# Optimization experiments

Hardware: AMD Instinct MI355X
Metric: run time of the kernel (lower is better)

The kernel has to match this reference:

```python
import jax, jax.numpy as jnp
import numpy as np

N = 50000      # nodes
E = 800000     # edges per relation
R = 4          # relations
F = 256        # feature_size
H = 128        # hid_dim
O = 32         # out_dim
B = 10000      # batch_nodes
EPS = 1e-5


def setup_inputs() -> dict:
    key = jax.random.key(0)
    ks = jax.random.split(key, 12)
    features = jax.random.normal(ks[0], (N, F), dtype=jnp.float32)
    multi_r_edge_index = jax.random.randint(ks[1], (R, 2, E), 0, N, dtype=jnp.int64)
    batch_nodes = jax.random.randint(ks[2], (B,), 0, N, dtype=jnp.int64)
    # per-relation params, stacked on leading R axis
    W1 = jax.random.normal(ks[3], (R, F, H), dtype=jnp.float32) / np.sqrt(F)
    b1 = jnp.zeros((R, H), dtype=jnp.float32)
    g1 = jnp.ones((R, H), dtype=jnp.float32)
    be1 = jnp.zeros((R, H), dtype=jnp.float32)
    W2 = jax.random.normal(ks[4], (R, H, O), dtype=jnp.float32) / np.sqrt(H)
    b2 = jnp.zeros((R, O), dtype=jnp.float32)
    g2 = jnp.ones((R, O), dtype=jnp.float32)
    be2 = jnp.zeros((R, O), dtype=jnp.float32)
    return {"features": features, "multi_r_edge_index": multi_r_edge_index,
            "batch_nodes": batch_nodes, "W1": W1, "b1": b1, "g1": g1, "be1": be1,
            "W2": W2, "b2": b2, "g2": g2, "be2": be2}


def gcn_conv(x, src, dst, W, b):
    # PyG GCNConv: h = x W; add self-loops; sym-norm aggregate; + bias
    h = x @ W                                   # [N, D]
    loops = jnp.arange(N, dtype=src.dtype)
    s = jnp.concatenate([src, loops])
    d = jnp.concatenate([dst, loops])
    deg = jax.ops.segment_sum(jnp.ones_like(d, dtype=h.dtype), d, num_segments=N)
    dinv = jnp.where(deg > 0, jax.lax.rsqrt(deg), 0.0)
    norm = dinv[s] * dinv[d]                    # [E+N]
    msgs = norm[:, None] * h[s]                 # gather [E+N, D]
    out = jax.ops.segment_sum(msgs, d, num_segments=N)  # scatter
    return out + b


def batchnorm(x, gamma, beta):
    # training-mode batch stats over node dim (biased variance)
    mean = jnp.mean(x, axis=0)
    var = jnp.mean(jnp.square(x - mean), axis=0)
    return gamma * (x - mean) * jax.lax.rsqrt(var + EPS) + beta


def reference(features, multi_r_edge_index, batch_nodes, W1, b1, g1, be1, W2, b2, g2, be2):
    embeds = []
    for i in range(R):  # small fixed loop over relations
        src = multi_r_edge_index[i, 0]
        dst = multi_r_edge_index[i, 1]
        x = gcn_conv(features, src, dst, W1[i], b1[i])
        x = jax.nn.relu(batchnorm(x, g1[i], be1[i]))
        # dropout: eval mode (identity)
        x = gcn_conv(x, src, dst, W2[i], b2[i])
        x = jax.nn.relu(batchnorm(x, g2[i], be2[i]))
        embeds.append(jax.nn.log_softmax(x[batch_nodes], axis=1))  # [B, O]
    multi = jnp.stack(embeds, axis=1)            # [B, R, O]
    return multi.reshape(B, R * O)
```

## Files before the change

kernel.cpp:

```cpp
#include <hip/hip_runtime.h>
#include <math.h>

#define NN 50000
#define EE 800000
#define RR 4
#define FF 256
#define HH 128
#define OO 32
#define BB 10000
#define EPSV 1e-5f
#define PAIR 2

#define NSEG 256
#define CH   (EE / NSEG)
#define NBK  256
#define BNODE 196
#define SCAP 36

typedef __bf16 bf16_t;
typedef __attribute__((ext_vector_type(8))) bf16_t bf16x8;
typedef __attribute__((ext_vector_type(4))) float f32x4;

__device__ __forceinline__ unsigned short f2bf(float f) {
    unsigned int u = __float_as_uint(f);
    u += 0x7fff + ((u >> 16) & 1);
    return (unsigned short)(u >> 16);
}
__device__ __forceinline__ float bf2f(unsigned short s) {
    return __uint_as_float(((unsigned int)s) << 16);
}
__device__ __forceinline__ void load_lds16(const void* g, void* l) {
    __builtin_amdgcn_global_load_lds(
        (const __attribute__((address_space(1))) unsigned int*)g,
        (__attribute__((address_space(3))) unsigned int*)l, 16, 0, 0);
}


__global__ void k_cvt_feat(const float* __restrict__ in, ushort* __restrict__ out) {
    int idx = blockIdx.x * 256 + threadIdx.x;
    const float4* p = (const float4*)in + (size_t)idx * 2;
    float4 a = p[0], b = p[1];
    uint4 o;
    o.x = (unsigned)f2bf(a.x) | ((unsigned)f2bf(a.y) << 16);
    o.y = (unsigned)f2bf(a.z) | ((unsigned)f2bf(a.w) << 16);
    o.z = (unsigned)f2bf(b.x) | ((unsigned)f2bf(b.y) << 16);
    o.w = (unsigned)f2bf(b.z) | ((unsigned)f2bf(b.w) << 16);
    ((uint4*)out)[idx] = o;
}

__global__ void k_cvt_w(const float* __restrict__ W1, const float* __restrict__ W2,
                        ushort* __restrict__ W1t, ushort* __restrict__ W2t) {
    int idx = blockIdx.x * 256 + threadIdx.x;
    if (idx < RR * FF * HH) {
        int r = idx >> 15, k = (idx >> 7) & 255, n = idx & 127;
        W1t[r * (HH * FF) + n * FF + k] = f2bf(W1[idx]);
    }
    if (idx < RR * HH * OO) {
        int r = idx >> 12, k = (idx >> 5) & 127, n = idx & 31;
        W2t[r * (OO * HH) + n * HH + k] = f2bf(W2[idx]);
    }
}


__global__ __launch_bounds__(256) void k_passA(const int* __restrict__ edges,
                                               uint* __restrict__ seg,
                                               int* __restrict__ cnt) {
    int r = blockIdx.y, blk = blockIdx.x, t = threadIdx.x;
    __shared__ int lcur[NBK];
    lcur[t] = 0;
    __syncthreads();
    const int* srcp = edges + (size_t)r * 2 * EE + blk * CH;
    const int* dstp = srcp + EE;
    uint* segbase = seg + (size_t)(r * NSEG + blk) * NBK * SCAP;
    for (int i = t; i < CH; i += 256) {
        int s = srcp[i], d = dstp[i];
        int b = d / BNODE;
        int dloc = d - b * BNODE;
        int pos = atomicAdd(&lcur[b], 1);
        if (pos < SCAP) segbase[b * SCAP + pos] = (uint)s | ((uint)dloc << 16);
    }
    __syncthreads();
    cnt[(r * NSEG + blk) * NBK + t] = min(lcur[t], SCAP);
}

__global__ void k_bbase(const int* __restrict__ cnt, int* __restrict__ bbase,
                        int* __restrict__ offs) {
    int r = blockIdx.x, t = threadIdx.x;
    int sum = 0;
    for (int s = 0; s < NSEG; ++s) sum += cnt[(r * NSEG + s) * NBK + t];
    __shared__ int sh[256];
    sh[t] = sum;
    __syncthreads();
    for (int off = 1; off < 256; off <<= 1) {
        int u = (t >= off) ? sh[t - off] : 0;
        __syncthreads();
        sh[t] += u;
        __syncthreads();
    }
    bbase[r * (NBK + 1) + t] = sh[t] - sum;
    if (t == 255) {
        bbase[r * (NBK + 1) + NBK] = sh[t];
        offs[r * (NN + 1) + NN] = sh[t];
    }
}

__global__ __launch_bounds__(256) void k_passB(const uint* __restrict__ seg,
                                               const int* __restrict__ cnt,
                                               const int* __restrict__ bbase,
                                               ushort* __restrict__ csr,
                                               int* __restrict__ offs,
                                               float* __restrict__ dinv) {
    int b = blockIdx.x, r = blockIdx.y, t = threadIdx.x;
    __shared__ int ldeg[256];
    __shared__ int lcur[256];
    __shared__ int sh[256];
    __shared__ int scnt[NSEG];
    ldeg[t] = 0;
    scnt[t] = cnt[(r * NSEG + t) * NBK + b];
    __syncthreads();
    const uint* segb = seg + (size_t)(r * NSEG) * NBK * SCAP + (size_t)b * SCAP;
    for (int idx = t; idx < NSEG * SCAP; idx += 256) {
        int s = idx / SCAP, i = idx - s * SCAP;
        if (i < scnt[s])
            atomicAdd(&ldeg[segb[(size_t)s * NBK * SCAP + i] >> 16], 1);
    }
    __syncthreads();
    int v = ldeg[t];
    sh[t] = v;
    __syncthreads();
    for (int off = 1; off < 256; off <<= 1) {
        int u = (t >= off) ? sh[t - off] : 0;
        __syncthreads();
        sh[t] += u;
        __syncthreads();
    }
    int ex = sh[t] - v;
    lcur[t] = ex;
    int gbase = bbase[r * (NBK + 1) + b];
    int n0 = b * BNODE;
    int n = n0 + t;
    if (t < BNODE && n < NN) {
        offs[r * (NN + 1) + n] = gbase + ex;
        dinv[r * NN + n] = rsqrtf((float)(v + 1));
    }
    __syncthreads();
    ushort* csrb = csr + (size_t)r * EE + gbase;
    for (int idx = t; idx < NSEG * SCAP; idx += 256) {
        int s = idx / SCAP, i = idx - s * SCAP;
        if (i < scnt[s]) {
            uint e = segb[(size_t)s * NBK * SCAP + i];
            int p = atomicAdd(&lcur[e >> 16], 1);
            csrb[p] = (ushort)(e & 0xffffu);
        }
    }
}


__global__ __launch_bounds__(256) void k_mm1(const ushort* __restrict__ A,
                                             const ushort* __restrict__ W1t_all,
                                             ushort* __restrict__ C_all, int rbase) {
    int pr = blockIdx.y, r = rbase + pr;
    const ushort* Wt = W1t_all + (size_t)r * FF * HH;
    ushort* C = C_all + (size_t)pr * NN * HH;
    __shared__ __align__(16) ushort As[128 * 32];
    __shared__ __align__(16) ushort Bs[128 * 32];
    int tid = threadIdx.x;
    int lane = tid & 63, w = tid >> 6;
    int wm = w >> 1, wn = w & 1;
    int row0 = blockIdx.x * 128;
    int l15 = lane & 15, l4 = lane >> 4;

    f32x4 acc[4][4];
#pragma unroll
    for (int mf = 0; mf < 4; ++mf)
#pragma unroll
        for (int nf = 0; nf < 4; ++nf) acc[mf][nf] = (f32x4)0.f;

    for (int k0 = 0; k0 < FF; k0 += 32) {
#pragma unroll
        for (int i = 0; i < 2; ++i) {
            int chunk = i * 256 + tid;
            int ar = chunk >> 2, as_ = chunk & 3;
            int grow = row0 + ar; if (grow > NN - 1) grow = NN - 1;
            load_lds16(A + (size_t)grow * FF + k0 + as_ * 8,
                       As + (size_t)(i * 256 + w * 64) * 8);
        }
#pragma unroll
        for (int i = 0; i < 2; ++i) {
            int chunk = i * 256 + tid;
            int bn = chunk >> 2, slot = chunk & 3;
            uint4 v = *(const uint4*)(Wt + bn * FF + k0 + slot * 8);
            int sw = slot ^ ((bn >> 1) & 3);
            *(uint4*)(Bs + bn * 32 + sw * 8) = v;
        }
        __syncthreads();
        bf16x8 af[4], bfr[4];
#pragma unroll
        for (int mf = 0; mf < 4; ++mf) {
            int row = wm * 64 + mf * 16 + l15;
            af[mf] = *(const bf16x8*)(As + row * 32 + l4 * 8);
        }
#pragma unroll
        for (int nf = 0; nf < 4; ++nf) {
            int n = wn * 64 + nf * 16 + l15;
            int sw = l4 ^ ((n >> 1) & 3);
            bfr[nf] = *(const bf16x8*)(Bs + n * 32 + sw * 8);
        }
#pragma unroll
        for (int mf = 0; mf < 4; ++mf)
#pragma unroll
            for (int nf = 0; nf < 4; ++nf)
                acc[mf][nf] = __builtin_amdgcn_mfma_f32_16x16x32_bf16(af[mf], bfr[nf], acc[mf][nf], 0, 0, 0);
        __syncthreads();
    }
#pragma unroll
    for (int mf = 0; mf < 4; ++mf) {
#pragma unroll
        for (int nf = 0; nf < 4; ++nf) {
#pragma unroll
            for (int j = 0; j < 4; ++j) {
                int row = row0 + wm * 64 + mf * 16 + l4 * 4 + j;
                if (row < NN)
                    C[(size_t)row * HH + wn * 64 + nf * 16 + l15] = f2bf(acc[mf][nf][j]);
            }
        }
    }
}


__global__ __launch_bounds__(256) void k_mm2(const ushort* __restrict__ A_all,
                                             const float* __restrict__ ab_all,
                                             const ushort* __restrict__ W2t_all,
                                             ushort* __restrict__ C_all, int rbase) {
    int pr = blockIdx.y, r = rbase + pr;
    const ushort* A = A_all + (size_t)pr * NN * HH;
    const float* ab = ab_all + pr * 2 * HH;
    const ushort* Wt = W2t_all + (size_t)r * OO * HH;
    ushort* C = C_all + (size_t)pr * NN * OO;
    __shared__ __align__(16) ushort As[256 * 32];
    __shared__ __align__(16) ushort Ws2[32 * 128];
    int tid = threadIdx.x;
    int lane = tid & 63, w = tid >> 6;
    int l15 = lane & 15, l4 = lane >> 4;
    int row0 = blockIdx.x * 256;

#pragma unroll
    for (int i = 0; i < 2; ++i) {
        int chunk = i * 256 + tid;
        int n = chunk >> 4, slot = chunk & 15;
        uint4 v = *(const uint4*)(Wt + n * HH + slot * 8);
        int sw = slot ^ (n & 7);
        *(uint4*)(Ws2 + n * HH + sw * 8) = v;
    }

    f32x4 acc[4][2];
#pragma unroll
    for (int mf = 0; mf < 4; ++mf)
#pragma unroll
        for (int nf = 0; nf < 2; ++nf) acc[mf][nf] = (f32x4)0.f;

    for (int k0 = 0; k0 < HH; k0 += 32) {
#pragma unroll
        for (int i = 0; i < 4; ++i) {
            int chunk = i * 256 + tid;
            int ar = chunk >> 2, cg = chunk & 3;
            int grow = row0 + ar; if (grow > NN - 1) grow = NN - 1;
            uint4 xv = *(const uint4*)(A + (size_t)grow * HH + k0 + cg * 8);
            const float* aa = ab + k0 + cg * 8;
            float4 a0 = *(const float4*)aa;
            float4 a1 = *(const float4*)(aa + 4);
            const float* bp = ab + HH + k0 + cg * 8;
            float4 b0 = *(const float4*)bp;
            float4 b1 = *(const float4*)(bp + 4);
            float y0 = fmaxf(a0.x * bf2f((ushort)(xv.x & 0xffff)) + b0.x, 0.f);
            float y1 = fmaxf(a0.y * bf2f((ushort)(xv.x >> 16)) + b0.y, 0.f);
            float y2 = fmaxf(a0.z * bf2f((ushort)(xv.y & 0xffff)) + b0.z, 0.f);
            float y3 = fmaxf(a0.w * bf2f((ushort)(xv.y >> 16)) + b0.w, 0.f);
            float y4 = fmaxf(a1.x * bf2f((ushort)(xv.z & 0xffff)) + b1.x, 0.f);
            float y5 = fmaxf(a1.y * bf2f((ushort)(xv.z >> 16)) + b1.y, 0.f);
            float y6 = fmaxf(a1.z * bf2f((ushort)(xv.w & 0xffff)) + b1.z, 0.f);
            float y7 = fmaxf(a1.w * bf2f((ushort)(xv.w >> 16)) + b1.w, 0.f);
            uint4 o;
            o.x = (unsigned)f2bf(y0) | ((unsigned)f2bf(y1) << 16);
            o.y = (unsigned)f2bf(y2) | ((unsigned)f2bf(y3) << 16);
            o.z = (unsigned)f2bf(y4) | ((unsigned)f2bf(y5) << 16);
            o.w = (unsigned)f2bf(y6) | ((unsigned)f2bf(y7) << 16);
            *(uint4*)(As + chunk * 8) = o;
        }
        __syncthreads();
        bf16x8 af[4], bfr[2];
#pragma unroll
        for (int mf = 0; mf < 4; ++mf)
            af[mf] = *(const bf16x8*)(As + (w * 64 + mf * 16 + l15) * 32 + l4 * 8);
#pragma unroll
        for (int nf = 0; nf < 2; ++nf) {
            int n = nf * 16 + l15;
            int slot = (k0 >> 3) + l4;
            int sw = slot ^ (n & 7);
            bfr[nf] = *(const bf16x8*)(Ws2 + n * HH + sw * 8);
        }
#pragma unroll
        for (int mf = 0; mf < 4; ++mf)
#pragma unroll
            for (int nf = 0; nf < 2; ++nf)
                acc[mf][nf] = __builtin_amdgcn_mfma_f32_16x16x32_bf16(af[mf], bfr[nf], acc[mf][nf], 0, 0, 0);
        __syncthreads();
    }
#pragma unroll
    for (int mf = 0; mf < 4; ++mf) {
#pragma unroll
        for (int nf = 0; nf < 2; ++nf) {
#pragma unroll
            for (int j = 0; j < 4; ++j) {
                int row = row0 + w * 64 + mf * 16 + l4 * 4 + j;
                if (row < NN)
                    C[(size_t)row * OO + nf * 16 + l15] = f2bf(acc[mf][nf][j]);
            }
        }
    }
}


__global__ void k_agg1(const ushort* __restrict__ X_all, ushort* __restrict__ Y_all,
                       const int* __restrict__ offs_all, const ushort* __restrict__ csr_all,
                       const float* __restrict__ dinv_all, int rbase) {
    int pr = blockIdx.y, r = rbase + pr;
    const uint* Xu = (const uint*)(X_all + (size_t)pr * NN * HH);
    uint* Yu = (uint*)(Y_all + (size_t)pr * NN * HH);
    const int* offs = offs_all + r * (NN + 1);
    const ushort* csr = csr_all + (size_t)r * EE;
    const float* dinv = dinv_all + (size_t)r * NN;
    int tid = threadIdx.x;
    int wid = tid >> 6, lane = tid & 63;
    int n = blockIdx.x * 4 + wid;
    if (n >= NN) return;
    float ax = 0.f, ay = 0.f;
    int e = offs[n], s1 = offs[n + 1];
    for (; e + 4 <= s1; e += 4) {
        int sa = csr[e], sb = csr[e + 1], sc = csr[e + 2], sd = csr[e + 3];
        uint va = Xu[sa * 64 + lane];
        uint vb = Xu[sb * 64 + lane];
        uint vc = Xu[sc * 64 + lane];
        uint vd = Xu[sd * 64 + lane];
        float wa = dinv[sa], wb = dinv[sb], wc = dinv[sc], wd = dinv[sd];
        ax += wa * bf2f((ushort)(va & 0xffff)); ay += wa * bf2f((ushort)(va >> 16));
        ax += wb * bf2f((ushort)(vb & 0xffff)); ay += wb * bf2f((ushort)(vb >> 16));
        ax += wc * bf2f((ushort)(vc & 0xffff)); ay += wc * bf2f((ushort)(vc >> 16));
        ax += wd * bf2f((ushort)(vd & 0xffff)); ay += wd * bf2f((ushort)(vd >> 16));
    }
    for (; e < s1; ++e) {
        int s = csr[e];
        float w = dinv[s];
        uint v = Xu[s * 64 + lane];
        ax += w * bf2f((ushort)(v & 0xffff)); ay += w * bf2f((ushort)(v >> 16));
    }
    float dn = dinv[n];
    uint v = Xu[n * 64 + lane];
    ax += dn * bf2f((ushort)(v & 0xffff));
    ay += dn * bf2f((ushort)(v >> 16));
    Yu[n * 64 + lane] = (uint)f2bf(ax * dn) | ((uint)f2bf(ay * dn) << 16);
}

__global__ void k_agg2(const ushort* __restrict__ X_all, ushort* __restrict__ Y_all,
                       const int* __restrict__ offs_all, const ushort* __restrict__ csr_all,
                       const float* __restrict__ dinv_all, int rbase) {
    int pr = blockIdx.y, r = rbase + pr;
    const ushort* X = X_all + (size_t)pr * NN * OO;
    ushort* Y = Y_all + (size_t)pr * NN * OO;
    const int* offs = offs_all + r * (NN + 1);
    const ushort* csr = csr_all + (size_t)r * EE;
    const float* dinv = dinv_all + (size_t)r * NN;
    int tid = threadIdx.x;
    int wid = tid >> 6, lane = tid & 63;
    int sub = lane >> 5, col = lane & 31;
    int n = blockIdx.x * 8 + wid * 2 + sub;
    if (n >= NN) return;
    float acc = 0.f;
    int e = offs[n], s1 = offs[n + 1];
    for (; e + 4 <= s1; e += 4) {
        int sa = csr[e], sb = csr[e + 1], sc = csr[e + 2], sd = csr[e + 3];
        float xa = bf2f(X[sa * OO + col]);
        float xb = bf2f(X[sb * OO + col]);
        float xc = bf2f(X[sc * OO + col]);
        float xd = bf2f(X[sd * OO + col]);
        acc += dinv[sa] * xa + dinv[sb] * xb + dinv[sc] * xc + dinv[sd] * xd;
    }
    for (; e < s1; ++e) {
        int s = csr[e];
        acc += dinv[s] * bf2f(X[s * OO + col]);
    }
    float dn = dinv[n];
    acc += dn * bf2f(X[n * OO + col]);
    Y[(size_t)n * OO + col] = f2bf(acc * dn);
}


template <int D>
__global__ void k_stats(const ushort* __restrict__ X_all, float* __restrict__ partial_all) {
    constexpr int BY = 256 / D;
    int pr = blockIdx.y;
    const ushort* X = X_all + (size_t)pr * NN * D;
    float* partial = partial_all + (size_t)pr * 256 * 2 * D;
    int c = threadIdx.x;
    int ty = threadIdx.y;
    float s = 0.f, ss = 0.f;
    for (int row = blockIdx.x * BY + ty; row < NN; row += 256 * BY) {
        float v = bf2f(X[(size_t)row * D + c]);
        s += v; ss += v * v;
    }
    __shared__ float ls[BY][D];
    __shared__ float lss[BY][D];
    ls[ty][c] = s; lss[ty][c] = ss;
    __syncthreads();
    if (ty == 0) {
#pragma unroll
        for (int y = 1; y < BY; ++y) { s += ls[y][c]; ss += lss[y][c]; }
        partial[blockIdx.x * 2 * D + c] = s;
        partial[blockIdx.x * 2 * D + D + c] = ss;
    }
}

template <int D>
__global__ void k_finalize(const float* __restrict__ partial_all, const float* __restrict__ g_all,
                           const float* __restrict__ be_all, float* __restrict__ ab_all, int rbase) {
    int pr = blockIdx.x, r = rbase + pr;
    const float* partial = partial_all + (size_t)pr * 256 * 2 * D;
    int c = threadIdx.x;
    float s = 0.f, ss = 0.f;
    for (int i = 0; i < 256; ++i) {
        s += partial[i * 2 * D + c];
        ss += partial[i * 2 * D + D + c];
    }
    float mean = s / (float)NN;
    float var = ss / (float)NN - mean * mean;
    float rstd = rsqrtf(var + EPSV);
    float a = g_all[r * D + c] * rstd;
    ab_all[pr * 2 * D + c] = a;
    ab_all[pr * 2 * D + D + c] = be_all[r * D + c] - mean * a;
}


__global__ void k_lsm(const ushort* __restrict__ X_all, const float* __restrict__ ab_all,
                      const int* __restrict__ batch, float* __restrict__ out, int rbase) {
    int pr = blockIdx.y, r = rbase + pr;
    const ushort* X = X_all + (size_t)pr * NN * OO;
    const float* ab = ab_all + pr * 2 * OO;
    int tx = threadIdx.x;
    int b = blockIdx.x * blockDim.y + threadIdx.y;
    if (b >= BB) return;
    int node = batch[b];
    float x = bf2f(X[(size_t)node * OO + tx]);
    float v = fmaxf(ab[tx] * x + ab[OO + tx], 0.f);
    float m = v;
#pragma unroll
    for (int off = 16; off; off >>= 1) m = fmaxf(m, __shfl_xor(m, off, 32));
    float e = expf(v - m);
    float sum = e;
#pragma unroll
    for (int off = 16; off; off >>= 1) sum += __shfl_xor(sum, off, 32);
    out[(size_t)b * (RR * OO) + r * OO + tx] = v - m - logf(sum);
}


extern "C" void kernel_launch(void* const* d_in, const int* in_sizes, int n_in,
                              void* d_out, int out_size, void* d_ws, size_t ws_size,
                              hipStream_t stream) {
    const float* features = (const float*)d_in[0];
    const int* edges = (const int*)d_in[1];
    const int* batch = (const int*)d_in[2];
    const float* W1 = (const float*)d_in[3];
    const float* g1 = (const float*)d_in[5];
    const float* be1 = (const float*)d_in[6];
    const float* W2 = (const float*)d_in[7];
    const float* g2 = (const float*)d_in[9];
    const float* be2 = (const float*)d_in[10];
    float* out = (float*)d_out;

    char* p = (char*)d_ws;
    auto carve = [&](size_t bytes) {
        void* q = (void*)p;
        p += (bytes + 255) & ~(size_t)255;
        return q;
    };
    ushort* Fbf = (ushort*)carve((size_t)NN * FF * 2);
    ushort* W1t = (ushort*)carve((size_t)RR * FF * HH * 2);
    ushort* W2t = (ushort*)carve((size_t)RR * HH * OO * 2);
    float* dinv = (float*)carve((size_t)RR * NN * 4);
    int* offs = (int*)carve((size_t)RR * (NN + 1) * 4);
    int* cnt = (int*)carve((size_t)RR * NSEG * NBK * 4);
    int* bbase = (int*)carve((size_t)RR * (NBK + 1) * 4);
    ushort* csr = (ushort*)carve((size_t)RR * EE * 2);
    ushort* bufAh = (ushort*)carve((size_t)PAIR * NN * HH * 2);
    ushort* bufB = (ushort*)carve((size_t)PAIR * NN * HH * 2);
    ushort* bufCh = (ushort*)carve((size_t)PAIR * NN * OO * 2);
    ushort* bufD = (ushort*)carve((size_t)PAIR * NN * OO * 2);
    float* partial = (float*)carve((size_t)PAIR * 256 * 2 * HH * 4);
    float* ab1 = (float*)carve((size_t)PAIR * 2 * HH * 4);
    float* ab2 = (float*)carve((size_t)PAIR * 2 * OO * 4);
    uint* seg = (uint*)bufAh;

    k_cvt_feat<<<NN * FF / 8 / 256, 256, 0, stream>>>(features, Fbf);
    k_cvt_w<<<(RR * FF * HH + 255) / 256, 256, 0, stream>>>(W1, W2, W1t, W2t);

    k_passA<<<dim3(NSEG, RR), 256, 0, stream>>>(edges, seg, cnt);
    k_bbase<<<RR, 256, 0, stream>>>(cnt, bbase, offs);
    k_passB<<<dim3(NBK, RR), 256, 0, stream>>>(seg, cnt, bbase, csr, offs, dinv);

    for (int rbase = 0; rbase < RR; rbase += PAIR) {
        k_mm1<<<dim3((NN + 127) / 128, PAIR), 256, 0, stream>>>(Fbf, W1t, bufAh, rbase);
        k_agg1<<<dim3((NN + 3) / 4, PAIR), 256, 0, stream>>>(bufAh, bufB, offs, csr, dinv, rbase);
        k_stats<HH><<<dim3(256, PAIR), dim3(HH, 2), 0, stream>>>(bufB, partial);
        k_finalize<HH><<<PAIR, HH, 0, stream>>>(partial, g1, be1, ab1, rbase);

        k_mm2<<<dim3((NN + 255) / 256, PAIR), 256, 0, stream>>>(bufB, ab1, W2t, bufCh, rbase);
        k_agg2<<<dim3((NN + 7) / 8, PAIR), 256, 0, stream>>>(bufCh, bufD, offs, csr, dinv, rbase);
        k_stats<OO><<<dim3(256, PAIR), dim3(OO, 8), 0, stream>>>(bufD, partial);
        k_finalize<OO><<<PAIR, OO, 0, stream>>>(partial, g2, be2, ab2, rbase);

        k_lsm<<<dim3((BB + 7) / 8, PAIR), dim3(32, 8), 0, stream>>>(bufD, ab2, batch, out, rbase);
    }
}
```

Before: 636.5 us.

## Process all relations at once when workspace allows, unroll gathers, vectorize stats

When the workspace is large enough, all four relations are processed in a single batch instead of two pairs. This halves the number of kernel launches and makes each grid larger, and the layer-2 buffers reuse the bf16 feature buffer once it is no longer needed. The aggregation kernels now gather eight neighbors per iteration to raise memory-level parallelism. The batch-norm stats kernel reads two bf16 values per 32-bit load. The larger batch needs more workspace and falls back to pairs otherwise; aliasing Fbf is only safe if k_mm1 for every relation has already run, which holds only when all four run in one batch.

```diff
diff --git a/kernel.cpp b/kernel.cpp
--- a/kernel.cpp
+++ b/kernel.cpp
@@ -9,7 +9,6 @@
 #define OO 32
 #define BB 10000
 #define EPSV 1e-5f
-#define PAIR 2
 
 #define NSEG 256
 #define CH   (EE / NSEG)
@@ -336,13 +335,29 @@
     if (n >= NN) return;
     float ax = 0.f, ay = 0.f;
     int e = offs[n], s1 = offs[n + 1];
+    for (; e + 8 <= s1; e += 8) {
+        int ia = csr[e], ib = csr[e + 1], ic = csr[e + 2], id = csr[e + 3];
+        int ie = csr[e + 4], if_ = csr[e + 5], ig = csr[e + 6], ih = csr[e + 7];
+        uint va = Xu[ia * 64 + lane], vb = Xu[ib * 64 + lane];
+        uint vc = Xu[ic * 64 + lane], vd = Xu[id * 64 + lane];
+        uint ve = Xu[ie * 64 + lane], vf = Xu[if_ * 64 + lane];
+        uint vg = Xu[ig * 64 + lane], vh = Xu[ih * 64 + lane];
+        float wa = dinv[ia], wb = dinv[ib], wc = dinv[ic], wd = dinv[id];
+        float we = dinv[ie], wf = dinv[if_], wg = dinv[ig], wh = dinv[ih];
+        ax += wa * bf2f((ushort)(va & 0xffff)); ay += wa * bf2f((ushort)(va >> 16));
+        ax += wb * bf2f((ushort)(vb & 0xffff)); ay += wb * bf2f((ushort)(vb >> 16));
+        ax += wc * bf2f((ushort)(vc & 0xffff)); ay += wc * bf2f((ushort)(vc >> 16));
+        ax += wd * bf2f((ushort)(vd & 0xffff)); ay += wd * bf2f((ushort)(vd >> 16));
+        ax += we * bf2f((ushort)(ve & 0xffff)); ay += we * bf2f((ushort)(ve >> 16));
+        ax += wf * bf2f((ushort)(vf & 0xffff)); ay += wf * bf2f((ushort)(vf >> 16));
+        ax += wg * bf2f((ushort)(vg & 0xffff)); ay += wg * bf2f((ushort)(vg >> 16));
+        ax += wh * bf2f((ushort)(vh & 0xffff)); ay += wh * bf2f((ushort)(vh >> 16));
+    }
     for (; e + 4 <= s1; e += 4) {
-        int sa = csr[e], sb = csr[e + 1], sc = csr[e + 2], sd = csr[e + 3];
-        uint va = Xu[sa * 64 + lane];
-        uint vb = Xu[sb * 64 + lane];
-        uint vc = Xu[sc * 64 + lane];
-        uint vd = Xu[sd * 64 + lane];
-        float wa = dinv[sa], wb = dinv[sb], wc = dinv[sc], wd = dinv[sd];
+        int ia = csr[e], ib = csr[e + 1], ic = csr[e + 2], id = csr[e + 3];
+        uint va = Xu[ia * 64 + lane], vb = Xu[ib * 64 + lane];
+        uint vc = Xu[ic * 64 + lane], vd = Xu[id * 64 + lane];
+        float wa = dinv[ia], wb = dinv[ib], wc = dinv[ic], wd = dinv[id];
         ax += wa * bf2f((ushort)(va & 0xffff)); ay += wa * bf2f((ushort)(va >> 16));
         ax += wb * bf2f((ushort)(vb & 0xffff)); ay += wb * bf2f((ushort)(vb >> 16));
         ax += wc * bf2f((ushort)(vc & 0xffff)); ay += wc * bf2f((ushort)(vc >> 16));
@@ -377,13 +392,21 @@
     if (n >= NN) return;
     float acc = 0.f;
     int e = offs[n], s1 = offs[n + 1];
+    for (; e + 8 <= s1; e += 8) {
+        int ia = csr[e], ib = csr[e + 1], ic = csr[e + 2], id = csr[e + 3];
+        int ie = csr[e + 4], if_ = csr[e + 5], ig = csr[e + 6], ih = csr[e + 7];
+        float xa = bf2f(X[ia * OO + col]), xb = bf2f(X[ib * OO + col]);
+        float xc = bf2f(X[ic * OO + col]), xd = bf2f(X[id * OO + col]);
+        float xe = bf2f(X[ie * OO + col]), xf = bf2f(X[if_ * OO + col]);
+        float xg = bf2f(X[ig * OO + col]), xh = bf2f(X[ih * OO + col]);
+        acc += dinv[ia] * xa + dinv[ib] * xb + dinv[ic] * xc + dinv[id] * xd;
+        acc += dinv[ie] * xe + dinv[if_] * xf + dinv[ig] * xg + dinv[ih] * xh;
+    }
     for (; e + 4 <= s1; e += 4) {
-        int sa = csr[e], sb = csr[e + 1], sc = csr[e + 2], sd = csr[e + 3];
-        float xa = bf2f(X[sa * OO + col]);
-        float xb = bf2f(X[sb * OO + col]);
-        float xc = bf2f(X[sc * OO + col]);
-        float xd = bf2f(X[sd * OO + col]);
-        acc += dinv[sa] * xa + dinv[sb] * xb + dinv[sc] * xc + dinv[sd] * xd;
+        int ia = csr[e], ib = csr[e + 1], ic = csr[e + 2], id = csr[e + 3];
+        float xa = bf2f(X[ia * OO + col]), xb = bf2f(X[ib * OO + col]);
+        float xc = bf2f(X[ic * OO + col]), xd = bf2f(X[id * OO + col]);
+        acc += dinv[ia] * xa + dinv[ib] * xb + dinv[ic] * xc + dinv[id] * xd;
     }
     for (; e < s1; ++e) {
         int s = csr[e];
@@ -397,26 +420,34 @@
 
 template <int D>
 __global__ void k_stats(const ushort* __restrict__ X_all, float* __restrict__ partial_all) {
-    constexpr int BY = 256 / D;
+    constexpr int CW = D / 2;
+    constexpr int BY = 512 / D;
     int pr = blockIdx.y;
-    const ushort* X = X_all + (size_t)pr * NN * D;
+    const uint* X = (const uint*)(X_all + (size_t)pr * NN * D);
     float* partial = partial_all + (size_t)pr * 256 * 2 * D;
     int c = threadIdx.x;
     int ty = threadIdx.y;
-    float s = 0.f, ss = 0.f;
+    float s0 = 0.f, ss0 = 0.f, s1 = 0.f, ss1 = 0.f;
     for (int row = blockIdx.x * BY + ty; row < NN; row += 256 * BY) {
-        float v = bf2f(X[(size_t)row * D + c]);
-        s += v; ss += v * v;
-    }
-    __shared__ float ls[BY][D];
-    __shared__ float lss[BY][D];
-    ls[ty][c] = s; lss[ty][c] = ss;
+        uint v = X[(size_t)row * CW + c];
+        float a = bf2f((ushort)(v & 0xffff)), b = bf2f((ushort)(v >> 16));
+        s0 += a; ss0 += a * a; s1 += b; ss1 += b * b;
+    }
+    __shared__ float ls[BY][2][CW];
+    __shared__ float lss[BY][2][CW];
+    ls[ty][0][c] = s0; ls[ty][1][c] = s1;
+    lss[ty][0][c] = ss0; lss[ty][1][c] = ss1;
     __syncthreads();
     if (ty == 0) {
 #pragma unroll
-        for (int y = 1; y < BY; ++y) { s += ls[y][c]; ss += lss[y][c]; }
-        partial[blockIdx.x * 2 * D + c] = s;
-        partial[blockIdx.x * 2 * D + D + c] = ss;
+        for (int y = 1; y < BY; ++y) {
+            s0 += ls[y][0][c]; s1 += ls[y][1][c];
+            ss0 += lss[y][0][c]; ss1 += lss[y][1][c];
+        }
+        partial[blockIdx.x * 2 * D + 2 * c] = s0;
+        partial[blockIdx.x * 2 * D + 2 * c + 1] = s1;
+        partial[blockIdx.x * 2 * D + D + 2 * c] = ss0;
+        partial[blockIdx.x * 2 * D + D + 2 * c + 1] = ss1;
     }
 }
 
@@ -490,13 +521,25 @@
     int* cnt = (int*)carve((size_t)RR * NSEG * NBK * 4);
     int* bbase = (int*)carve((size_t)RR * (NBK + 1) * 4);
     ushort* csr = (ushort*)carve((size_t)RR * EE * 2);
-    ushort* bufAh = (ushort*)carve((size_t)PAIR * NN * HH * 2);
-    ushort* bufB = (ushort*)carve((size_t)PAIR * NN * HH * 2);
-    ushort* bufCh = (ushort*)carve((size_t)PAIR * NN * OO * 2);
-    ushort* bufD = (ushort*)carve((size_t)PAIR * NN * OO * 2);
-    float* partial = (float*)carve((size_t)PAIR * 256 * 2 * HH * 4);
-    float* ab1 = (float*)carve((size_t)PAIR * 2 * HH * 4);
-    float* ab2 = (float*)carve((size_t)PAIR * 2 * OO * 4);
+
+    size_t fixed = (size_t)(p - (char*)d_ws);
+    size_t need4 = fixed + 2 * (size_t)4 * NN * HH * 2 + (size_t)4 * 256 * 2 * HH * 4 + (1 << 20);
+    int PR = (ws_size >= need4) ? 4 : 2;
+
+    ushort* bufAh = (ushort*)carve((size_t)PR * NN * HH * 2);
+    ushort* bufB = (ushort*)carve((size_t)PR * NN * HH * 2);
+    ushort* bufCh;
+    ushort* bufD;
+    if (PR == 4) {
+        bufCh = Fbf;
+        bufD = Fbf + (size_t)4 * NN * OO;
+    } else {
+        bufCh = (ushort*)carve((size_t)PR * NN * OO * 2);
+        bufD = (ushort*)carve((size_t)PR * NN * OO * 2);
+    }
+    float* partial = (float*)carve((size_t)PR * 256 * 2 * HH * 4);
+    float* ab1 = (float*)carve((size_t)PR * 2 * HH * 4);
+    float* ab2 = (float*)carve((size_t)PR * 2 * OO * 4);
     uint* seg = (uint*)bufAh;
 
     k_cvt_feat<<<NN * FF / 8 / 256, 256, 0, stream>>>(features, Fbf);
@@ -506,17 +549,17 @@
     k_bbase<<<RR, 256, 0, stream>>>(cnt, bbase, offs);
     k_passB<<<dim3(NBK, RR), 256, 0, stream>>>(seg, cnt, bbase, csr, offs, dinv);
 
-    for (int rbase = 0; rbase < RR; rbase += PAIR) {
-        k_mm1<<<dim3((NN + 127) / 128, PAIR), 256, 0, stream>>>(Fbf, W1t, bufAh, rbase);
-        k_agg1<<<dim3((NN + 3) / 4, PAIR), 256, 0, stream>>>(bufAh, bufB, offs, csr, dinv, rbase);
-        k_stats<HH><<<dim3(256, PAIR), dim3(HH, 2), 0, stream>>>(bufB, partial);
-        k_finalize<HH><<<PAIR, HH, 0, stream>>>(partial, g1, be1, ab1, rbase);
-
-        k_mm2<<<dim3((NN + 255) / 256, PAIR), 256, 0, stream>>>(bufB, ab1, W2t, bufCh, rbase);
-        k_agg2<<<dim3((NN + 7) / 8, PAIR), 256, 0, stream>>>(bufCh, bufD, offs, csr, dinv, rbase);
-        k_stats<OO><<<dim3(256, PAIR), dim3(OO, 8), 0, stream>>>(bufD, partial);
-        k_finalize<OO><<<PAIR, OO, 0, stream>>>(partial, g2, be2, ab2, rbase);
-
-        k_lsm<<<dim3((BB + 7) / 8, PAIR), dim3(32, 8), 0, stream>>>(bufD, ab2, batch, out, rbase);
-    }
-}
+    for (int rbase = 0; rbase < RR; rbase += PR) {
+        k_mm1<<<dim3((NN + 127) / 128, PR), 256, 0, stream>>>(Fbf, W1t, bufAh, rbase);
+        k_agg1<<<dim3((NN + 3) / 4, PR), 256, 0, stream>>>(bufAh, bufB, offs, csr, dinv, rbase);
+        k_stats<HH><<<dim3(256, PR), dim3(HH / 2, 512 / HH), 0, stream>>>(bufB, partial);
+        k_finalize<HH><<<PR, HH, 0, stream>>>(partial, g1, be1, ab1, rbase);
+
+        k_mm2<<<dim3((NN + 255) / 256, PR), 256, 0, stream>>>(bufB, ab1, W2t, bufCh, rbase);
+        k_agg2<<<dim3((NN + 7) / 8, PR), 256, 0, stream>>>(bufCh, bufD, offs, csr, dinv, rbase);
+        k_stats<OO><<<dim3(256, PR), dim3(OO / 2, 512 / OO), 0, stream>>>(bufD, partial);
+        k_finalize<OO><<<PR, OO, 0, stream>>>(partial, g2, be2, ab2, rbase);
+
+        k_lsm<<<dim3((BB + 7) / 8, PR), dim3(32, 8), 0, stream>>>(bufD, ab2, batch, out, rbase);
+    }
+}
```

Measured after the change: 520.1 us. 18.3% less time.
